# Kernel optimization log

Hardware: AMD Instinct MI355X
Metric: run time of the kernel (lower is better)

Reference implementation:

```python
import jax, jax.numpy as jnp
import numpy as np

D = 512  # feature_dim


def setup_inputs() -> dict:
    key = jax.random.key(0)
    ks = jax.random.split(key, 10)
    s = 1.0 / np.sqrt(D)
    s2 = 1.0 / np.sqrt(2 * D)
    return {
        "X": jax.random.normal(ks[0], (8, 2048, D), dtype=jnp.float32),
        "Y": jax.random.normal(ks[1], (8, 2048, D), dtype=jnp.float32),
        "W_xq": jax.random.uniform(ks[2], (D, D), jnp.float32, -s, s),
        "b_xq": jax.random.uniform(ks[3], (D,), jnp.float32, -s, s),
        "W_yq": jax.random.uniform(ks[4], (D, D), jnp.float32, -s, s),
        "b_yq": jax.random.uniform(ks[5], (D,), jnp.float32, -s, s),
        "W_fk": jax.random.uniform(ks[6], (D, 2 * D), jnp.float32, -s2, s2),
        "b_fk": jax.random.uniform(ks[7], (D,), jnp.float32, -s2, s2),
        "W_fv": jax.random.uniform(ks[8], (D, 2 * D), jnp.float32, -s2, s2),
        "b_fv": jax.random.uniform(ks[9], (D,), jnp.float32, -s2, s2),
    }


def reference(X, Y, W_xq, b_xq, W_yq, b_yq, W_fk, b_fk, W_fv, b_fv):
    # Dropout is evaluated in eval mode (identity).
    scale = 1.0 / jnp.sqrt(jnp.asarray(D, X.dtype))
    Q1 = jnp.einsum('bsd,ed->bse', X, W_xq) + b_xq  # [B,S,D]
    Q2 = jnp.einsum('bsd,ed->bse', Y, W_yq) + b_yq
    Q_cat = jnp.concatenate([Q1, Q2], axis=-1)      # [B,S,2D]
    K_f = jnp.einsum('bsc,ec->bse', Q_cat, W_fk) + b_fk
    V_f = jnp.einsum('bsc,ec->bse', Q_cat, W_fv) + b_fv

    def attend(Q):
        scores = jnp.einsum('bqd,bkd->bqk', Q, K_f) * scale  # [B,S,S]
        A = jax.nn.softmax(scores, axis=-1)
        return jnp.einsum('bqk,bkd->bqd', A, V_f)

    U_A1 = X + attend(Q1)
    U_A2 = Y + attend(Q2)
    return U_A1 + U_A2
```

## Files before the change

kernel.cpp:

```cpp
#include <hip/hip_runtime.h>


#define B_    8
#define S_    2048
#define D_    512
#define M_TOT (B_ * S_)

typedef __bf16 bf16_t;
typedef __bf16 bf16x8 __attribute__((ext_vector_type(8)));
typedef __bf16 bf16x4 __attribute__((ext_vector_type(4)));
typedef float  f32x4  __attribute__((ext_vector_type(4)));

typedef __attribute__((address_space(1))) const void* gas_cv;
typedef __attribute__((address_space(3))) void*       las_v;

__device__ __forceinline__ f32x4 mfma16(bf16x8 a, bf16x8 b, f32x4 c) {
    return __builtin_amdgcn_mfma_f32_16x16x32_bf16(a, b, c, 0, 0, 0);
}
__device__ __forceinline__ void load_lds16(const void* g, void* l) {
    __builtin_amdgcn_global_load_lds((gas_cv)g, (las_v)l, 16, 0, 0);
}

__global__ __launch_bounds__(256) void k_qgemm(
    const float* __restrict__ X, const float* __restrict__ Y,
    const float* __restrict__ Wxq, const float* __restrict__ bxq,
    const float* __restrict__ Wyq, const float* __restrict__ byq,
    bf16_t* __restrict__ Qcat)
{
    __shared__ __attribute__((aligned(16))) bf16_t Al[128 * 40];
    __shared__ __attribute__((aligned(16))) bf16_t Bl[128 * 40];
    const int m0 = blockIdx.x * 128;
    const int n0 = blockIdx.y * 128;
    const bool second = (n0 >= 512);
    const float* A    = second ? Y : X;
    const float* W    = second ? Wyq : Wxq;
    const float* bias = second ? byq : bxq;
    const int nw = n0 & 511;
    const int t    = threadIdx.x;
    const int lane = t & 63;
    const int wv   = t >> 6;
    const int wm   = (wv & 1) * 64;
    const int wn   = (wv >> 1) * 64;
    const int l15  = lane & 15;
    const int quad = lane >> 4;

    f32x4 acc[4][4] = {};

    for (int k0 = 0; k0 < 512; k0 += 32) {
        __syncthreads();
#pragma unroll
        for (int p = 0; p < 4; ++p) {
            const int lin = p * 256 + t;
            const int row = lin >> 3;
            const int ch  = (lin & 7) * 4;
            const float4 va = *(const float4*)(A + (size_t)(m0 + row) * 512 + k0 + ch);
            bf16x4 pa = { (bf16_t)va.x, (bf16_t)va.y, (bf16_t)va.z, (bf16_t)va.w };
            *(bf16x4*)(Al + row * 40 + ch) = pa;
            const float4 vb = *(const float4*)(W + (size_t)(nw + row) * 512 + k0 + ch);
            bf16x4 pb = { (bf16_t)vb.x, (bf16_t)vb.y, (bf16_t)vb.z, (bf16_t)vb.w };
            *(bf16x4*)(Bl + row * 40 + ch) = pb;
        }
        __syncthreads();
        bf16x8 af[4], bfr[4];
#pragma unroll
        for (int i = 0; i < 4; ++i)
            af[i] = *(const bf16x8*)(Al + (wm + i * 16 + l15) * 40 + quad * 8);
#pragma unroll
        for (int i = 0; i < 4; ++i)
            bfr[i] = *(const bf16x8*)(Bl + (wn + i * 16 + l15) * 40 + quad * 8);
#pragma unroll
        for (int mt = 0; mt < 4; ++mt)
#pragma unroll
            for (int nt = 0; nt < 4; ++nt)
                acc[mt][nt] = mfma16(af[mt], bfr[nt], acc[mt][nt]);
    }

#pragma unroll
    for (int nt = 0; nt < 4; ++nt) {
        const int col  = n0 + wn + nt * 16 + l15;
        const float bv = bias[col & 511];
#pragma unroll
        for (int mt = 0; mt < 4; ++mt) {
            const int rowb = m0 + wm + mt * 16 + quad * 4;
#pragma unroll
            for (int r = 0; r < 4; ++r)
                Qcat[(size_t)(rowb + r) * 1024 + col] = (bf16_t)(acc[mt][nt][r] + bv);
        }
    }
}

__global__ __launch_bounds__(256) void k_kvgemm(
    const bf16_t* __restrict__ Qcat,
    const float* __restrict__ Wfk, const float* __restrict__ bfk,
    const float* __restrict__ Wfv, const float* __restrict__ bfv,
    bf16_t* __restrict__ Kf, bf16_t* __restrict__ Vt)
{
    __shared__ __attribute__((aligned(16))) union {
        struct { bf16_t Al[128 * 40]; bf16_t Bl[128 * 40]; } g;
        bf16_t T[128 * 132];
    } sm;
    const int m0 = blockIdx.x * 128;
    const int n0 = blockIdx.y * 128;
    const bool isV = (n0 >= 512);
    const float* W    = isV ? Wfv : Wfk;
    const float* bias = isV ? bfv : bfk;
    const int nw = n0 & 511;
    const int t    = threadIdx.x;
    const int lane = t & 63;
    const int wv   = t >> 6;
    const int wm   = (wv & 1) * 64;
    const int wn   = (wv >> 1) * 64;
    const int l15  = lane & 15;
    const int quad = lane >> 4;

    f32x4 acc[4][4] = {};

    for (int k0 = 0; k0 < 1024; k0 += 32) {
        __syncthreads();
#pragma unroll
        for (int p = 0; p < 2; ++p) {
            const int lin = p * 256 + t;
            const int row = lin >> 2;
            const int ch  = (lin & 3) * 8;
            *(bf16x8*)(sm.g.Al + row * 40 + ch) =
                *(const bf16x8*)(Qcat + (size_t)(m0 + row) * 1024 + k0 + ch);
        }
#pragma unroll
        for (int p = 0; p < 4; ++p) {
            const int lin = p * 256 + t;
            const int row = lin >> 3;
            const int ch  = (lin & 7) * 4;
            const float4 vb = *(const float4*)(W + (size_t)(nw + row) * 1024 + k0 + ch);
            bf16x4 pb = { (bf16_t)vb.x, (bf16_t)vb.y, (bf16_t)vb.z, (bf16_t)vb.w };
            *(bf16x4*)(sm.g.Bl + row * 40 + ch) = pb;
        }
        __syncthreads();
        bf16x8 af[4], bfr[4];
#pragma unroll
        for (int i = 0; i < 4; ++i)
            af[i] = *(const bf16x8*)(sm.g.Al + (wm + i * 16 + l15) * 40 + quad * 8);
#pragma unroll
        for (int i = 0; i < 4; ++i)
            bfr[i] = *(const bf16x8*)(sm.g.Bl + (wn + i * 16 + l15) * 40 + quad * 8);
#pragma unroll
        for (int mt = 0; mt < 4; ++mt)
#pragma unroll
            for (int nt = 0; nt < 4; ++nt)
                acc[mt][nt] = mfma16(af[mt], bfr[nt], acc[mt][nt]);
    }

    if (!isV) {
#pragma unroll
        for (int nt = 0; nt < 4; ++nt) {
            const int col  = n0 + wn + nt * 16 + l15;
            const float bv = bias[col];
#pragma unroll
            for (int mt = 0; mt < 4; ++mt) {
                const int rowb = m0 + wm + mt * 16 + quad * 4;
#pragma unroll
                for (int r = 0; r < 4; ++r)
                    Kf[(size_t)(rowb + r) * 512 + col] = (bf16_t)(acc[mt][nt][r] + bv);
            }
        }
    } else {
        __syncthreads();
#pragma unroll
        for (int nt = 0; nt < 4; ++nt) {
            const int dl = wn + nt * 16 + l15;
            const float bv = bias[nw + dl];
#pragma unroll
            for (int mt = 0; mt < 4; ++mt) {
                const int sl = wm + mt * 16 + quad * 4;
#pragma unroll
                for (int r = 0; r < 4; ++r)
                    sm.T[dl * 132 + sl + r] = (bf16_t)(acc[mt][nt][r] + bv);
            }
        }
        __syncthreads();
        const int bb = m0 >> 11;
        const int sb = m0 & 2047;
        const int half = lane >> 5;
        const int sl4  = (lane & 31) * 4;
#pragma unroll
        for (int i = 0; i < 16; ++i) {
            const int dl = wv * 32 + i * 2 + half;
            const bf16x4 v = *(const bf16x4*)(sm.T + dl * 132 + sl4);
            *(bf16x4*)(Vt + (size_t)(bb * 512 + nw + dl) * 2048 + sb + sl4) = v;
        }
    }
}

__global__ __launch_bounds__(256, 2) void k_attn(
    const bf16_t* __restrict__ Qcat, const bf16_t* __restrict__ Kf,
    const bf16_t* __restrict__ Vt,
    const float* __restrict__ X, const float* __restrict__ Y,
    float* __restrict__ out, bf16_t* __restrict__ attn,
    const int mode, const int which)
{
    __shared__ __attribute__((aligned(16))) bf16_t Kl[2][32 * 520];
    __shared__ __attribute__((aligned(16))) bf16_t Pl[2][64 * 40];
    __shared__ float lsumL[64];

    const int b = blockIdx.y;
    const int w = (mode == 0) ? (int)blockIdx.z : which;
    const int t    = threadIdx.x;
    const int lane = t & 63;
    const int wv   = t >> 6;
    const int l15  = lane & 15;
    const int quad = lane >> 4;
    const int q0   = blockIdx.x * 64;
    const int qw   = q0 + wv * 16;

    const bf16_t* Kbase = Kf + (size_t)b * S_ * 512;
    const bf16_t* Vbase = Vt + ((size_t)b * 512 + wv * 128) * S_;

    bf16x8 aq[16];
    {
        const bf16_t* qp = Qcat + (size_t)(b * S_ + qw + l15) * 1024 + w * 512 + quad * 8;
#pragma unroll
        for (int ks = 0; ks < 16; ++ks) aq[ks] = *(const bf16x8*)(qp + ks * 32);
    }

    f32x4 acc[4][8] = {};
    float lacc[4] = { 0.f, 0.f, 0.f, 0.f };
    const float sc2 = 0.04419417382415922f * 1.4426950408889634f;

#pragma unroll
    for (int p = 0; p < 8; ++p) {
        const int row = wv * 8 + p;
        load_lds16(Kbase + (size_t)row * 512 + lane * 8, Kl[0] + row * 520);
    }
    __syncthreads();

    {
#pragma unroll
        for (int p = 0; p < 8; ++p) {
            const int row = wv * 8 + p;
            load_lds16(Kbase + (size_t)(32 + row) * 512 + lane * 8, Kl[1] + row * 520);
        }
        f32x4 s0a = {}, s0b = {}, s1a = {}, s1b = {};
#pragma unroll
        for (int ks = 0; ks < 16; ks += 2) {
            const bf16x8 b0 = *(const bf16x8*)(Kl[0] + l15 * 520 + ks * 32 + quad * 8);
            const bf16x8 b1 = *(const bf16x8*)(Kl[0] + (16 + l15) * 520 + ks * 32 + quad * 8);
            const bf16x8 c0 = *(const bf16x8*)(Kl[0] + l15 * 520 + (ks + 1) * 32 + quad * 8);
            const bf16x8 c1 = *(const bf16x8*)(Kl[0] + (16 + l15) * 520 + (ks + 1) * 32 + quad * 8);
            s0a = mfma16(aq[ks], b0, s0a);
            s1a = mfma16(aq[ks], b1, s1a);
            s0b = mfma16(aq[ks + 1], c0, s0b);
            s1b = mfma16(aq[ks + 1], c1, s1b);
        }
        const f32x4 sA = s0a + s0b, sB = s1a + s1b;
#pragma unroll
        for (int r = 0; r < 4; ++r) {
            const float p0 = exp2f(sA[r] * sc2);
            const float p1 = exp2f(sB[r] * sc2);
            lacc[r] += p0 + p1;
            Pl[0][(wv * 16 + quad * 4 + r) * 40 + l15] = (bf16_t)p0;
            Pl[0][(wv * 16 + quad * 4 + r) * 40 + 16 + l15] = (bf16_t)p1;
        }
        __syncthreads();
    }

    for (int kb = 1; kb < 64; ++kb) {
        const int cur = kb & 1;
        const int prv = cur ^ 1;

        {
            const bf16_t* src = Kbase + (size_t)(kb + 1) * 32 * 512;
#pragma unroll
            for (int p = 0; p < 8; ++p) {
                const int row = wv * 8 + p;
                load_lds16(src + (size_t)row * 512 + lane * 8, Kl[prv] + row * 520);
            }
        }

        bf16x8 vb[8];
#pragma unroll
        for (int i = 0; i < 8; ++i)
            vb[i] = *(const bf16x8*)(Vbase + (size_t)(i * 16 + l15) * S_ +
                                     (kb - 1) * 32 + quad * 8);

        f32x4 s0a = {}, s0b = {}, s1a = {}, s1b = {};
#pragma unroll
        for (int ks = 0; ks < 16; ks += 2) {
            const bf16x8 b0 = *(const bf16x8*)(Kl[cur] + l15 * 520 + ks * 32 + quad * 8);
            const bf16x8 b1 = *(const bf16x8*)(Kl[cur] + (16 + l15) * 520 + ks * 32 + quad * 8);
            const bf16x8 c0 = *(const bf16x8*)(Kl[cur] + l15 * 520 + (ks + 1) * 32 + quad * 8);
            const bf16x8 c1 = *(const bf16x8*)(Kl[cur] + (16 + l15) * 520 + (ks + 1) * 32 + quad * 8);
            s0a = mfma16(aq[ks], b0, s0a);
            s1a = mfma16(aq[ks], b1, s1a);
            s0b = mfma16(aq[ks + 1], c0, s0b);
            s1b = mfma16(aq[ks + 1], c1, s1b);
        }

        {
            bf16x8 ap[4];
#pragma unroll
            for (int qt = 0; qt < 4; ++qt)
                ap[qt] = *(const bf16x8*)(Pl[prv] + (qt * 16 + l15) * 40 + quad * 8);
#pragma unroll
            for (int dt = 0; dt < 8; ++dt)
#pragma unroll
                for (int qt = 0; qt < 4; ++qt)
                    acc[qt][dt] = mfma16(ap[qt], vb[dt], acc[qt][dt]);
        }

        const f32x4 sA = s0a + s0b, sB = s1a + s1b;
#pragma unroll
        for (int r = 0; r < 4; ++r) {
            const float p0 = exp2f(sA[r] * sc2);
            const float p1 = exp2f(sB[r] * sc2);
            lacc[r] += p0 + p1;
            Pl[cur][(wv * 16 + quad * 4 + r) * 40 + l15] = (bf16_t)p0;
            Pl[cur][(wv * 16 + quad * 4 + r) * 40 + 16 + l15] = (bf16_t)p1;
        }

        __syncthreads();
    }

    {
        bf16x8 vb[8];
#pragma unroll
        for (int i = 0; i < 8; ++i)
            vb[i] = *(const bf16x8*)(Vbase + (size_t)(i * 16 + l15) * S_ +
                                     63 * 32 + quad * 8);
        bf16x8 ap[4];
#pragma unroll
        for (int qt = 0; qt < 4; ++qt)
            ap[qt] = *(const bf16x8*)(Pl[1] + (qt * 16 + l15) * 40 + quad * 8);
#pragma unroll
        for (int dt = 0; dt < 8; ++dt)
#pragma unroll
            for (int qt = 0; qt < 4; ++qt)
                acc[qt][dt] = mfma16(ap[qt], vb[dt], acc[qt][dt]);
    }

    {
        float lrow[4];
#pragma unroll
        for (int r = 0; r < 4; ++r) {
            float v = lacc[r];
#pragma unroll
            for (int off = 1; off < 16; off <<= 1) v += __shfl_xor(v, off, 64);
            lrow[r] = v;
        }
        if (l15 == 0) {
#pragma unroll
            for (int r = 0; r < 4; ++r) lsumL[wv * 16 + quad * 4 + r] = lrow[r];
        }
    }
    __syncthreads();

#pragma unroll
    for (int qt = 0; qt < 4; ++qt) {
        f32x4 inv;
#pragma unroll
        for (int r = 0; r < 4; ++r) inv[r] = 1.0f / lsumL[qt * 16 + quad * 4 + r];
#pragma unroll
        for (int dt = 0; dt < 8; ++dt) {
            const int d = wv * 128 + dt * 16 + l15;
#pragma unroll
            for (int r = 0; r < 4; ++r) {
                const float v = acc[qt][dt][r] * inv[r];
                const size_t idx =
                    (size_t)(b * S_ + q0 + qt * 16 + quad * 4 + r) * 512 + d;
                if (mode == 0)      attn[(size_t)w * M_TOT * 512 + idx] = (bf16_t)v;
                else if (mode == 1) out[idx] = X[idx] + Y[idx] + v;
                else                out[idx] += v;
            }
        }
    }
}

__global__ __launch_bounds__(256) void k_add(
    const float* __restrict__ X, const float* __restrict__ Y,
    const bf16_t* __restrict__ a0, const bf16_t* __restrict__ a1,
    float* __restrict__ out)
{
    const size_t i = ((size_t)blockIdx.x * 256 + threadIdx.x) * 4;
    const float4 x = *(const float4*)(X + i);
    const float4 y = *(const float4*)(Y + i);
    const bf16x4 v0 = *(const bf16x4*)(a0 + i);
    const bf16x4 v1 = *(const bf16x4*)(a1 + i);
    float4 o;
    o.x = x.x + y.x + (float)v0[0] + (float)v1[0];
    o.y = x.y + y.y + (float)v0[1] + (float)v1[1];
    o.z = x.z + y.z + (float)v0[2] + (float)v1[2];
    o.w = x.w + y.w + (float)v0[3] + (float)v1[3];
    *(float4*)(out + i) = o;
}

extern "C" void kernel_launch(void* const* d_in, const int* in_sizes, int n_in,
                              void* d_out, int out_size, void* d_ws, size_t ws_size,
                              hipStream_t stream)
{
    const float* X   = (const float*)d_in[0];
    const float* Y   = (const float*)d_in[1];
    const float* Wxq = (const float*)d_in[2];
    const float* bxq = (const float*)d_in[3];
    const float* Wyq = (const float*)d_in[4];
    const float* byq = (const float*)d_in[5];
    const float* Wfk = (const float*)d_in[6];
    const float* bfk = (const float*)d_in[7];
    const float* Wfv = (const float*)d_in[8];
    const float* bfv = (const float*)d_in[9];
    float* out = (float*)d_out;
    char*  ws  = (char*)d_ws;

    bf16_t* Qcat = (bf16_t*)(ws);
    bf16_t* Kf   = (bf16_t*)(ws + (size_t)33554432);
    bf16_t* Vt   = (bf16_t*)(ws + (size_t)50331648);
    bf16_t* attn = (bf16_t*)(ws + (size_t)67108864);
    const bool big = ws_size >= (size_t)100663296;

    k_qgemm<<<dim3(128, 8), 256, 0, stream>>>(X, Y, Wxq, bxq, Wyq, byq, Qcat);
    k_kvgemm<<<dim3(128, 8), 256, 0, stream>>>(Qcat, Wfk, bfk, Wfv, bfv, Kf, Vt);
    if (big) {
        k_attn<<<dim3(32, 8, 2), 256, 0, stream>>>(Qcat, Kf, Vt, X, Y, out, attn, 0, 0);
        k_add<<<dim3(8192), 256, 0, stream>>>(X, Y, attn, attn + (size_t)M_TOT * 512, out);
    } else {
        k_attn<<<dim3(32, 8, 1), 256, 0, stream>>>(Qcat, Kf, Vt, X, Y, out, attn, 1, 0);
        k_attn<<<dim3(32, 8, 1), 256, 0, stream>>>(Qcat, Kf, Vt, X, Y, out, attn, 2, 1);
    }
}
```

Before: 475.9 us.

## Warp-specialize attention kernel into QK/softmax producers and PV consumer waves

The attention block grows to six waves. Two producer waves compute QK^T scores, exponentiate and write P tiles to LDS. Four consumer waves prefetch K tiles and run the P·V MFMAs plus the epilogue. The aim is to overlap softmax and score work with the PV matmul across specialized waves instead of serializing them inside each wave. In exchange, producer waves hold twice as many Q fragments, register pressure changes under the (384,2) bounds, and the QK work now sits on fewer waves, so it may become the bottleneck.

```diff
diff --git a/kernel.cpp b/kernel.cpp
--- a/kernel.cpp
+++ b/kernel.cpp
@@ -190,7 +190,7 @@
     }
 }
 
-__global__ __launch_bounds__(256, 2) void k_attn(
+__global__ __launch_bounds__(384, 2) void k_attn(
     const bf16_t* __restrict__ Qcat, const bf16_t* __restrict__ Kf,
     const bf16_t* __restrict__ Vt,
     const float* __restrict__ X, const float* __restrict__ Y,
@@ -209,92 +209,107 @@
     const int l15  = lane & 15;
     const int quad = lane >> 4;
     const int q0   = blockIdx.x * 64;
-    const int qw   = q0 + wv * 16;
+    const bool prod = (wv < 2);
+    const int p  = wv;
+    const int cv = wv - 2;
 
     const bf16_t* Kbase = Kf + (size_t)b * S_ * 512;
-    const bf16_t* Vbase = Vt + ((size_t)b * 512 + wv * 128) * S_;
-
-    bf16x8 aq[16];
-    {
-        const bf16_t* qp = Qcat + (size_t)(b * S_ + qw + l15) * 1024 + w * 512 + quad * 8;
-#pragma unroll
-        for (int ks = 0; ks < 16; ++ks) aq[ks] = *(const bf16x8*)(qp + ks * 32);
+    const bf16_t* Vbase = Vt + ((size_t)b * 512 + cv * 128) * S_;
+
+    const float sc2 = 0.04419417382415922f * 1.4426950408889634f;
+
+    bf16x8 aq[2][16];
+    f32x4  lacc[2] = {};
+    if (prod) {
+        const bf16_t* qp = Qcat + (size_t)(b * S_ + q0 + p * 32 + l15) * 1024
+                         + w * 512 + quad * 8;
+#pragma unroll
+        for (int qt = 0; qt < 2; ++qt)
+#pragma unroll
+            for (int ks = 0; ks < 16; ++ks)
+                aq[qt][ks] = *(const bf16x8*)(qp + qt * 16 * 1024 + ks * 32);
     }
 
     f32x4 acc[4][8] = {};
-    float lacc[4] = { 0.f, 0.f, 0.f, 0.f };
-    const float sc2 = 0.04419417382415922f * 1.4426950408889634f;
-
-#pragma unroll
-    for (int p = 0; p < 8; ++p) {
-        const int row = wv * 8 + p;
-        load_lds16(Kbase + (size_t)row * 512 + lane * 8, Kl[0] + row * 520);
+
+    if (!prod) {
+#pragma unroll
+        for (int i = 0; i < 8; ++i) {
+            const int row = cv * 8 + i;
+            load_lds16(Kbase + (size_t)row * 512 + lane * 8, Kl[0] + row * 520);
+        }
     }
     __syncthreads();
 
-    {
-#pragma unroll
-        for (int p = 0; p < 8; ++p) {
-            const int row = wv * 8 + p;
+    if (prod) {
+        f32x4 s[2][2] = {};
+#pragma unroll
+        for (int ks = 0; ks < 16; ++ks) {
+            const bf16x8 bk0 = *(const bf16x8*)(Kl[0] + l15 * 520 + ks * 32 + quad * 8);
+            const bf16x8 bk1 = *(const bf16x8*)(Kl[0] + (16 + l15) * 520 + ks * 32 + quad * 8);
+            s[0][0] = mfma16(aq[0][ks], bk0, s[0][0]);
+            s[0][1] = mfma16(aq[0][ks], bk1, s[0][1]);
+            s[1][0] = mfma16(aq[1][ks], bk0, s[1][0]);
+            s[1][1] = mfma16(aq[1][ks], bk1, s[1][1]);
+        }
+#pragma unroll
+        for (int qt = 0; qt < 2; ++qt)
+#pragma unroll
+            for (int r = 0; r < 4; ++r) {
+                const float p0 = exp2f(s[qt][0][r] * sc2);
+                const float p1 = exp2f(s[qt][1][r] * sc2);
+                lacc[qt][r] += p0 + p1;
+                const int row = p * 32 + qt * 16 + quad * 4 + r;
+                Pl[0][row * 40 + l15] = (bf16_t)p0;
+                Pl[0][row * 40 + 16 + l15] = (bf16_t)p1;
+            }
+    } else {
+#pragma unroll
+        for (int i = 0; i < 8; ++i) {
+            const int row = cv * 8 + i;
             load_lds16(Kbase + (size_t)(32 + row) * 512 + lane * 8, Kl[1] + row * 520);
         }
-        f32x4 s0a = {}, s0b = {}, s1a = {}, s1b = {};
-#pragma unroll
-        for (int ks = 0; ks < 16; ks += 2) {
-            const bf16x8 b0 = *(const bf16x8*)(Kl[0] + l15 * 520 + ks * 32 + quad * 8);
-            const bf16x8 b1 = *(const bf16x8*)(Kl[0] + (16 + l15) * 520 + ks * 32 + quad * 8);
-            const bf16x8 c0 = *(const bf16x8*)(Kl[0] + l15 * 520 + (ks + 1) * 32 + quad * 8);
-            const bf16x8 c1 = *(const bf16x8*)(Kl[0] + (16 + l15) * 520 + (ks + 1) * 32 + quad * 8);
-            s0a = mfma16(aq[ks], b0, s0a);
-            s1a = mfma16(aq[ks], b1, s1a);
-            s0b = mfma16(aq[ks + 1], c0, s0b);
-            s1b = mfma16(aq[ks + 1], c1, s1b);
-        }
-        const f32x4 sA = s0a + s0b, sB = s1a + s1b;
-#pragma unroll
-        for (int r = 0; r < 4; ++r) {
-            const float p0 = exp2f(sA[r] * sc2);
-            const float p1 = exp2f(sB[r] * sc2);
-            lacc[r] += p0 + p1;
-            Pl[0][(wv * 16 + quad * 4 + r) * 40 + l15] = (bf16_t)p0;
-            Pl[0][(wv * 16 + quad * 4 + r) * 40 + 16 + l15] = (bf16_t)p1;
-        }
-        __syncthreads();
-    }
+    }
+    __syncthreads();
 
     for (int kb = 1; kb < 64; ++kb) {
         const int cur = kb & 1;
         const int prv = cur ^ 1;
 
-        {
+        if (prod) {
+            f32x4 s[2][2] = {};
+#pragma unroll
+            for (int ks = 0; ks < 16; ++ks) {
+                const bf16x8 bk0 = *(const bf16x8*)(Kl[cur] + l15 * 520 + ks * 32 + quad * 8);
+                const bf16x8 bk1 = *(const bf16x8*)(Kl[cur] + (16 + l15) * 520 + ks * 32 + quad * 8);
+                s[0][0] = mfma16(aq[0][ks], bk0, s[0][0]);
+                s[0][1] = mfma16(aq[0][ks], bk1, s[0][1]);
+                s[1][0] = mfma16(aq[1][ks], bk0, s[1][0]);
+                s[1][1] = mfma16(aq[1][ks], bk1, s[1][1]);
+            }
+#pragma unroll
+            for (int qt = 0; qt < 2; ++qt)
+#pragma unroll
+                for (int r = 0; r < 4; ++r) {
+                    const float p0 = exp2f(s[qt][0][r] * sc2);
+                    const float p1 = exp2f(s[qt][1][r] * sc2);
+                    lacc[qt][r] += p0 + p1;
+                    const int row = p * 32 + qt * 16 + quad * 4 + r;
+                    Pl[cur][row * 40 + l15] = (bf16_t)p0;
+                    Pl[cur][row * 40 + 16 + l15] = (bf16_t)p1;
+                }
+        } else {
             const bf16_t* src = Kbase + (size_t)(kb + 1) * 32 * 512;
 #pragma unroll
-            for (int p = 0; p < 8; ++p) {
-                const int row = wv * 8 + p;
+            for (int i = 0; i < 8; ++i) {
+                const int row = cv * 8 + i;
                 load_lds16(src + (size_t)row * 512 + lane * 8, Kl[prv] + row * 520);
             }
-        }
-
-        bf16x8 vb[8];
-#pragma unroll
-        for (int i = 0; i < 8; ++i)
-            vb[i] = *(const bf16x8*)(Vbase + (size_t)(i * 16 + l15) * S_ +
-                                     (kb - 1) * 32 + quad * 8);
-
-        f32x4 s0a = {}, s0b = {}, s1a = {}, s1b = {};
-#pragma unroll
-        for (int ks = 0; ks < 16; ks += 2) {
-            const bf16x8 b0 = *(const bf16x8*)(Kl[cur] + l15 * 520 + ks * 32 + quad * 8);
-            const bf16x8 b1 = *(const bf16x8*)(Kl[cur] + (16 + l15) * 520 + ks * 32 + quad * 8);
-            const bf16x8 c0 = *(const bf16x8*)(Kl[cur] + l15 * 520 + (ks + 1) * 32 + quad * 8);
-            const bf16x8 c1 = *(const bf16x8*)(Kl[cur] + (16 + l15) * 520 + (ks + 1) * 32 + quad * 8);
-            s0a = mfma16(aq[ks], b0, s0a);
-            s1a = mfma16(aq[ks], b1, s1a);
-            s0b = mfma16(aq[ks + 1], c0, s0b);
-            s1b = mfma16(aq[ks + 1], c1, s1b);
-        }
-
-        {
+            bf16x8 vb[8];
+#pragma unroll
+            for (int i = 0; i < 8; ++i)
+                vb[i] = *(const bf16x8*)(Vbase + (size_t)(i * 16 + l15) * S_ +
+                                         (kb - 1) * 32 + quad * 8);
             bf16x8 ap[4];
 #pragma unroll
             for (int qt = 0; qt < 4; ++qt)
@@ -306,20 +321,24 @@
                     acc[qt][dt] = mfma16(ap[qt], vb[dt], acc[qt][dt]);
         }
 
-        const f32x4 sA = s0a + s0b, sB = s1a + s1b;
-#pragma unroll
-        for (int r = 0; r < 4; ++r) {
-            const float p0 = exp2f(sA[r] * sc2);
-            const float p1 = exp2f(sB[r] * sc2);
-            lacc[r] += p0 + p1;
-            Pl[cur][(wv * 16 + quad * 4 + r) * 40 + l15] = (bf16_t)p0;
-            Pl[cur][(wv * 16 + quad * 4 + r) * 40 + 16 + l15] = (bf16_t)p1;
-        }
-
-        __syncthreads();
-    }
-
-    {
+        __syncthreads();
+    }
+
+    if (prod) {
+#pragma unroll
+        for (int qt = 0; qt < 2; ++qt) {
+#pragma unroll
+            for (int r = 0; r < 4; ++r) {
+                float v = lacc[qt][r];
+#pragma unroll
+                for (int off = 1; off < 16; off <<= 1) v += __shfl_xor(v, off, 64);
+                if (l15 == 0) lsumL[p * 32 + qt * 16 + quad * 4 + r] = v;
+            }
+        }
+    }
+    __syncthreads();
+
+    if (!prod) {
         bf16x8 vb[8];
 #pragma unroll
         for (int i = 0; i < 8; ++i)
@@ -334,40 +353,24 @@
 #pragma unroll
             for (int qt = 0; qt < 4; ++qt)
                 acc[qt][dt] = mfma16(ap[qt], vb[dt], acc[qt][dt]);
-    }
-
-    {
-        float lrow[4];
-#pragma unroll
-        for (int r = 0; r < 4; ++r) {
-            float v = lacc[r];
-#pragma unroll
-            for (int off = 1; off < 16; off <<= 1) v += __shfl_xor(v, off, 64);
-            lrow[r] = v;
-        }
-        if (l15 == 0) {
-#pragma unroll
-            for (int r = 0; r < 4; ++r) lsumL[wv * 16 + quad * 4 + r] = lrow[r];
-        }
-    }
-    __syncthreads();
-
-#pragma unroll
-    for (int qt = 0; qt < 4; ++qt) {
-        f32x4 inv;
-#pragma unroll
-        for (int r = 0; r < 4; ++r) inv[r] = 1.0f / lsumL[qt * 16 + quad * 4 + r];
-#pragma unroll
-        for (int dt = 0; dt < 8; ++dt) {
-            const int d = wv * 128 + dt * 16 + l15;
-#pragma unroll
-            for (int r = 0; r < 4; ++r) {
-                const float v = acc[qt][dt][r] * inv[r];
-                const size_t idx =
-                    (size_t)(b * S_ + q0 + qt * 16 + quad * 4 + r) * 512 + d;
-                if (mode == 0)      attn[(size_t)w * M_TOT * 512 + idx] = (bf16_t)v;
-                else if (mode == 1) out[idx] = X[idx] + Y[idx] + v;
-                else                out[idx] += v;
+
+#pragma unroll
+        for (int qt = 0; qt < 4; ++qt) {
+            f32x4 inv;
+#pragma unroll
+            for (int r = 0; r < 4; ++r) inv[r] = 1.0f / lsumL[qt * 16 + quad * 4 + r];
+#pragma unroll
+            for (int dt = 0; dt < 8; ++dt) {
+                const int d = cv * 128 + dt * 16 + l15;
+#pragma unroll
+                for (int r = 0; r < 4; ++r) {
+                    const float v = acc[qt][dt][r] * inv[r];
+                    const size_t idx =
+                        (size_t)(b * S_ + q0 + qt * 16 + quad * 4 + r) * 512 + d;
+                    if (mode == 0)      attn[(size_t)w * M_TOT * 512 + idx] = (bf16_t)v;
+                    else if (mode == 1) out[idx] = X[idx] + Y[idx] + v;
+                    else                out[idx] += v;
+                }
             }
         }
     }
@@ -417,10 +420,10 @@
     k_qgemm<<<dim3(128, 8), 256, 0, stream>>>(X, Y, Wxq, bxq, Wyq, byq, Qcat);
     k_kvgemm<<<dim3(128, 8), 256, 0, stream>>>(Qcat, Wfk, bfk, Wfv, bfv, Kf, Vt);
     if (big) {
-        k_attn<<<dim3(32, 8, 2), 256, 0, stream>>>(Qcat, Kf, Vt, X, Y, out, attn, 0, 0);
+        k_attn<<<dim3(32, 8, 2), 384, 0, stream>>>(Qcat, Kf, Vt, X, Y, out, attn, 0, 0);
         k_add<<<dim3(8192), 256, 0, stream>>>(X, Y, attn, attn + (size_t)M_TOT * 512, out);
     } else {
-        k_attn<<<dim3(32, 8, 1), 256, 0, stream>>>(Qcat, Kf, Vt, X, Y, out, attn, 1, 0);
-        k_attn<<<dim3(32, 8, 1), 256, 0, stream>>>(Qcat, Kf, Vt, X, Y, out, attn, 2, 1);
-    }
-}
+        k_attn<<<dim3(32, 8, 1), 384, 0, stream>>>(Qcat, Kf, Vt, X, Y, out, attn, 1, 0);
+        k_attn<<<dim3(32, 8, 1), 384, 0, stream>>>(Qcat, Kf, Vt, X, Y, out, attn, 2, 1);
+    }
+}
```

Result: slower. 755.1 us (+58.7%).
